# Optimization experiments

Hardware: AMD Instinct MI355X
Metric: run time of the kernel (lower is better)

Reference implementation:

```python
import jax, jax.numpy as jnp
import numpy as np

N, D, S = 8192, 1024, 16
EPS = 1e-5

def setup_inputs() -> dict:
    key = jax.random.key(0)
    ks = jax.random.split(key, 11)
    return {
        "x_t":   jax.random.normal(ks[0], (N, D), dtype=jnp.float32),
        "state": jax.random.normal(ks[1], (N, D, S), dtype=jnp.float32),
        "log_A": jax.random.normal(ks[2], (D, S), dtype=jnp.float32) * 0.1,
        "B":     jax.random.normal(ks[3], (D, S), dtype=jnp.float32) * 0.1,
        "C":     jax.random.normal(ks[4], (D, S), dtype=jnp.float32) * 0.1,
        "Wd":    jax.random.normal(ks[5], (D, D), dtype=jnp.float32) * (1.0 / np.sqrt(D)),
        "bd":    jnp.zeros((D,), dtype=jnp.float32),
        "Wg":    jax.random.normal(ks[6], (D, D), dtype=jnp.float32) * (1.0 / np.sqrt(D)),
        "bg":    jnp.zeros((D,), dtype=jnp.float32),
        "gamma": jnp.ones((D,), dtype=jnp.float32),
        "beta":  jnp.zeros((D,), dtype=jnp.float32),
    }

def reference(x_t, state, log_A, B, C, Wd, bd, Wg, bg, gamma, beta):
    # delta_proj: Linear + Softplus  -> [n, d]
    delta = jax.nn.softplus(x_t @ Wd.T + bd)
    # continuous A and exp discretization -> [n, d, s]
    A_cont = -jnp.exp(log_A)
    A_disc = jnp.exp(delta[:, :, None] * A_cont[None])
    # B_disc * x_t[..., None] == (delta * x_t)[:, :, None] * B
    new_state = A_disc * state + (delta * x_t)[:, :, None] * B[None]
    # contract tiny state dim s=16 -> [n, d]
    out = jnp.einsum('nds,ds->nd', new_state, C)
    gate = jax.nn.silu(x_t @ Wg.T + bg)
    residual = x_t + gate * out
    # LayerNorm (biased variance, eps=1e-5, affine)
    mu = jnp.mean(residual, axis=-1, keepdims=True)
    var = jnp.mean(jnp.square(residual - mu), axis=-1, keepdims=True)
    y = (residual - mu) / jnp.sqrt(var + EPS) * gamma + beta
    return (y, new_state)
```

## Files before the change

kernel.cpp:

```cpp
#include <hip/hip_runtime.h>

#define N_ROWS 8192
#define DIM 1024
#define S_DIM 16

typedef __attribute__((ext_vector_type(8))) __bf16 bf16x8;
typedef __attribute__((ext_vector_type(4))) float f32x4;

__device__ __forceinline__ unsigned short f2bf(float f) {
  union { float f; unsigned u; } v; v.f = f;
  unsigned r = v.u + 0x7FFFu + ((v.u >> 16) & 1u);
  return (unsigned short)(r >> 16);
}
__device__ __forceinline__ float bf2f(unsigned short b) {
  union { unsigned u; float f; } v; v.u = ((unsigned)b) << 16;
  return v.f;
}

__global__ void cvt_bf16_k(const float* __restrict__ src,
                           unsigned short* __restrict__ dst, int n4) {
  int i = blockIdx.x * blockDim.x + threadIdx.x;
  if (i >= n4) return;
  float4 v = ((const float4*)src)[i];
  ushort4 o;
  o.x = f2bf(v.x); o.y = f2bf(v.y); o.z = f2bf(v.z); o.w = f2bf(v.w);
  ((ushort4*)dst)[i] = o;
}

__global__ void acont_k(const float* __restrict__ la, float* __restrict__ ac, int n) {
  int i = blockIdx.x * blockDim.x + threadIdx.x;
  if (i < n) ac[i] = -__expf(la[i]);
}

__global__ __launch_bounds__(256) void gemm_act_k(
    const unsigned short* __restrict__ X,
    const unsigned short* __restrict__ W,
    const float* __restrict__ bias,
    unsigned short* __restrict__ outdg,
    int act)
{
  __shared__ unsigned short As[128][40];
  __shared__ unsigned short Bs[128][40];

  const int tid  = threadIdx.x;
  const int lane = tid & 63;
  const int wave = tid >> 6;
  const int qr = (wave >> 1) * 64;
  const int qc = (wave & 1) * 64;
  const int bj = blockIdx.x * 128;
  const int bn = blockIdx.y * 128;

  f32x4 acc[4][4];
  #pragma unroll
  for (int i = 0; i < 4; i++)
    #pragma unroll
    for (int j = 0; j < 4; j++)
      acc[i][j] = (f32x4){0.f, 0.f, 0.f, 0.f};

  const int sr = tid >> 2;
  const int so = (tid & 3) * 8;
  const unsigned short* Xa = X + (size_t)(bn + sr) * DIM + so;
  const unsigned short* Xb = X + (size_t)(bn + sr + 64) * DIM + so;
  const unsigned short* Wa = W + (size_t)(bj + sr) * DIM + so;
  const unsigned short* Wb = W + (size_t)(bj + sr + 64) * DIM + so;

  const int rl = lane & 15;
  const int kq = (lane >> 4) * 8;

  for (int k0 = 0; k0 < DIM; k0 += 32) {
    int4 a0 = *(const int4*)(Xa + k0);
    int4 a1 = *(const int4*)(Xb + k0);
    int4 b0 = *(const int4*)(Wa + k0);
    int4 b1 = *(const int4*)(Wb + k0);
    __syncthreads();
    *(int4*)&As[sr][so]      = a0;
    *(int4*)&As[sr + 64][so] = a1;
    *(int4*)&Bs[sr][so]      = b0;
    *(int4*)&Bs[sr + 64][so] = b1;
    __syncthreads();

    bf16x8 af[4], bfr[4];
    #pragma unroll
    for (int i = 0; i < 4; i++) af[i]  = *(const bf16x8*)&As[qr + i * 16 + rl][kq];
    #pragma unroll
    for (int j = 0; j < 4; j++) bfr[j] = *(const bf16x8*)&Bs[qc + j * 16 + rl][kq];

    #pragma unroll
    for (int i = 0; i < 4; i++)
      #pragma unroll
      for (int j = 0; j < 4; j++)
        acc[i][j] = __builtin_amdgcn_mfma_f32_16x16x32_bf16(af[i], bfr[j], acc[i][j], 0, 0, 0);
  }

  #pragma unroll
  for (int i = 0; i < 4; i++) {
    const int rowb = bn + qr + i * 16 + (lane >> 4) * 4;
    #pragma unroll
    for (int j = 0; j < 4; j++) {
      const int col = bj + qc + j * 16 + rl;
      const float bia = bias[col];
      #pragma unroll
      for (int r = 0; r < 4; r++) {
        float v = acc[i][j][r] + bia;
        float o;
        if (act == 0) o = (v > 20.f) ? v : log1pf(__expf(v));
        else          o = v / (1.f + __expf(-v));
        outdg[(size_t)(rowb + r) * 2048 + act * 1024 + col] = f2bf(o);
      }
    }
  }
}

__global__ __launch_bounds__(256) void state_ln_k(
    const float* __restrict__ x,
    const float* __restrict__ state,
    const float* __restrict__ acont,
    const float* __restrict__ Bm,
    const float* __restrict__ Cm,
    const float* __restrict__ gamma,
    const float* __restrict__ beta,
    float* __restrict__ y,
    float* __restrict__ ns)
{
  const int n = blockIdx.x;
  const int tid = threadIdx.x;
  const unsigned short* dg = (const unsigned short*)(y + (size_t)n * DIM);

  float res[4];
  #pragma unroll
  for (int q = 0; q < 4; q++) {
    const int d = tid + q * 256;
    const size_t nd = (size_t)n * DIM + d;
    const float xd = x[nd];
    const float dl = bf2f(dg[d]);
    const float gt = bf2f(dg[DIM + d]);
    const float dx = dl * xd;

    const float4* st = (const float4*)(state + nd * S_DIM);
    float4*       no = (float4*)(ns + nd * S_DIM);
    const float4* a4 = (const float4*)(acont + d * S_DIM);
    const float4* b4 = (const float4*)(Bm + d * S_DIM);
    const float4* c4 = (const float4*)(Cm + d * S_DIM);

    float accv = 0.f;
    #pragma unroll
    for (int s = 0; s < 4; s++) {
      float4 sv = st[s], av = a4[s], bv = b4[s], cv = c4[s];
      float4 o;
      o.x = __expf(dl * av.x) * sv.x + dx * bv.x;
      o.y = __expf(dl * av.y) * sv.y + dx * bv.y;
      o.z = __expf(dl * av.z) * sv.z + dx * bv.z;
      o.w = __expf(dl * av.w) * sv.w + dx * bv.w;
      accv += o.x * cv.x + o.y * cv.y + o.z * cv.z + o.w * cv.w;
      no[s] = o;
    }
    res[q] = xd + gt * accv;
  }

  float s1 = res[0] + res[1] + res[2] + res[3];
  float s2 = res[0] * res[0] + res[1] * res[1] + res[2] * res[2] + res[3] * res[3];
  #pragma unroll
  for (int off = 32; off > 0; off >>= 1) {
    s1 += __shfl_down(s1, off, 64);
    s2 += __shfl_down(s2, off, 64);
  }
  __shared__ float red[8];
  if ((tid & 63) == 0) { red[tid >> 6] = s1; red[4 + (tid >> 6)] = s2; }
  __syncthreads();
  const float t1 = red[0] + red[1] + red[2] + red[3];
  const float t2 = red[4] + red[5] + red[6] + red[7];
  const float mu = t1 * (1.f / (float)DIM);
  const float var = t2 * (1.f / (float)DIM) - mu * mu;
  const float rstd = rsqrtf(var + 1e-5f);

  #pragma unroll
  for (int q = 0; q < 4; q++) {
    const int d = tid + q * 256;
    y[(size_t)n * DIM + d] = (res[q] - mu) * rstd * gamma[d] + beta[d];
  }
}

extern "C" void kernel_launch(void* const* d_in, const int* in_sizes, int n_in,
                              void* d_out, int out_size, void* d_ws, size_t ws_size,
                              hipStream_t stream) {
  const float* x     = (const float*)d_in[0];
  const float* state = (const float*)d_in[1];
  const float* logA  = (const float*)d_in[2];
  const float* Bm    = (const float*)d_in[3];
  const float* Cm    = (const float*)d_in[4];
  const float* Wd    = (const float*)d_in[5];
  const float* bd    = (const float*)d_in[6];
  const float* Wg    = (const float*)d_in[7];
  const float* bg    = (const float*)d_in[8];
  const float* gamma = (const float*)d_in[9];
  const float* beta  = (const float*)d_in[10];

  float* y  = (float*)d_out;
  float* ns = (float*)d_out + (size_t)N_ROWS * DIM;

  unsigned short* xb  = (unsigned short*)d_ws;
  unsigned short* wdb = xb + (size_t)N_ROWS * DIM;
  unsigned short* wgb = wdb + (size_t)DIM * DIM;
  float* acont = (float*)(wgb + (size_t)DIM * DIM);

  hipLaunchKernelGGL(cvt_bf16_k, dim3(8192), dim3(256), 0, stream, x, xb, N_ROWS * DIM / 4);
  hipLaunchKernelGGL(cvt_bf16_k, dim3(1024), dim3(256), 0, stream, Wd, wdb, DIM * DIM / 4);
  hipLaunchKernelGGL(cvt_bf16_k, dim3(1024), dim3(256), 0, stream, Wg, wgb, DIM * DIM / 4);
  hipLaunchKernelGGL(acont_k, dim3(64), dim3(256), 0, stream, logA, acont, DIM * S_DIM);

  hipLaunchKernelGGL(gemm_act_k, dim3(8, 64), dim3(256), 0, stream, xb, wdb, bd,
                     (unsigned short*)y, 0);
  hipLaunchKernelGGL(gemm_act_k, dim3(8, 64), dim3(256), 0, stream, xb, wgb, bg,
                     (unsigned short*)y, 1);

  hipLaunchKernelGGL(state_ln_k, dim3(N_ROWS), dim3(256), 0, stream,
                     x, state, acont, Bm, Cm, gamma, beta, y, ns);
}
```

Baseline: 1.259 ms.

## Coalesce state access with four lanes per channel and merge the two GEMM launches

```diff
diff --git a/kernel.cpp b/kernel.cpp
--- a/kernel.cpp
+++ b/kernel.cpp
@@ -35,9 +35,9 @@
 __global__ __launch_bounds__(256) void gemm_act_k(
     const unsigned short* __restrict__ X,
     const unsigned short* __restrict__ W,
-    const float* __restrict__ bias,
-    unsigned short* __restrict__ outdg,
-    int act)
+    const float* __restrict__ bias_d,
+    const float* __restrict__ bias_g,
+    unsigned short* __restrict__ outdg)
 {
   __shared__ unsigned short As[128][40];
   __shared__ unsigned short Bs[128][40];
@@ -49,6 +49,7 @@
   const int qc = (wave & 1) * 64;
   const int bj = blockIdx.x * 128;
   const int bn = blockIdx.y * 128;
+  const int actq = (bj >= 1024);
 
   f32x4 acc[4][4];
   #pragma unroll
@@ -97,15 +98,15 @@
     const int rowb = bn + qr + i * 16 + (lane >> 4) * 4;
     #pragma unroll
     for (int j = 0; j < 4; j++) {
-      const int col = bj + qc + j * 16 + rl;
-      const float bia = bias[col];
+      const int colp = bj + qc + j * 16 + rl;
+      const float bia = actq ? bias_g[colp - 1024] : bias_d[colp];
       #pragma unroll
       for (int r = 0; r < 4; r++) {
         float v = acc[i][j][r] + bia;
         float o;
-        if (act == 0) o = (v > 20.f) ? v : log1pf(__expf(v));
-        else          o = v / (1.f + __expf(-v));
-        outdg[(size_t)(rowb + r) * 2048 + act * 1024 + col] = f2bf(o);
+        if (!actq) o = (v > 20.f) ? v : log1pf(__expf(v));
+        else       o = v / (1.f + __expf(-v));
+        outdg[(size_t)(rowb + r) * 2048 + colp] = f2bf(o);
       }
     }
   }
@@ -126,45 +127,58 @@
   const int tid = threadIdx.x;
   const unsigned short* dg = (const unsigned short*)(y + (size_t)n * DIM);
 
-  float res[4];
-  #pragma unroll
-  for (int q = 0; q < 4; q++) {
-    const int d = tid + q * 256;
+  const int sc  = tid & 3;
+  const int dl4 = tid >> 2;
+
+  __shared__ float rbuf[DIM];
+  __shared__ float red[8];
+
+  const float4* st4 = (const float4*)state;
+  float4*       ns4 = (float4*)ns;
+  const float4* a4  = (const float4*)acont;
+  const float4* b4  = (const float4*)Bm;
+  const float4* c4  = (const float4*)Cm;
+
+  float s1 = 0.f, s2 = 0.f;
+  const float lnmask = (sc == 0) ? 1.f : 0.f;
+
+  #pragma unroll 2
+  for (int q = 0; q < 16; q++) {
+    const int d = q * 64 + dl4;
     const size_t nd = (size_t)n * DIM + d;
+
     const float xd = x[nd];
     const float dl = bf2f(dg[d]);
     const float gt = bf2f(dg[DIM + d]);
     const float dx = dl * xd;
 
-    const float4* st = (const float4*)(state + nd * S_DIM);
-    float4*       no = (float4*)(ns + nd * S_DIM);
-    const float4* a4 = (const float4*)(acont + d * S_DIM);
-    const float4* b4 = (const float4*)(Bm + d * S_DIM);
-    const float4* c4 = (const float4*)(Cm + d * S_DIM);
-
-    float accv = 0.f;
-    #pragma unroll
-    for (int s = 0; s < 4; s++) {
-      float4 sv = st[s], av = a4[s], bv = b4[s], cv = c4[s];
-      float4 o;
-      o.x = __expf(dl * av.x) * sv.x + dx * bv.x;
-      o.y = __expf(dl * av.y) * sv.y + dx * bv.y;
-      o.z = __expf(dl * av.z) * sv.z + dx * bv.z;
-      o.w = __expf(dl * av.w) * sv.w + dx * bv.w;
-      accv += o.x * cv.x + o.y * cv.y + o.z * cv.z + o.w * cv.w;
-      no[s] = o;
-    }
-    res[q] = xd + gt * accv;
-  }
-
-  float s1 = res[0] + res[1] + res[2] + res[3];
-  float s2 = res[0] * res[0] + res[1] * res[1] + res[2] * res[2] + res[3] * res[3];
+    float4 sv = st4[nd * 4 + sc];
+    float4 av = a4[(size_t)d * 4 + sc];
+    float4 bv = b4[(size_t)d * 4 + sc];
+    float4 cv = c4[(size_t)d * 4 + sc];
+
+    float4 o;
+    o.x = __expf(dl * av.x) * sv.x + dx * bv.x;
+    o.y = __expf(dl * av.y) * sv.y + dx * bv.y;
+    o.z = __expf(dl * av.z) * sv.z + dx * bv.z;
+    o.w = __expf(dl * av.w) * sv.w + dx * bv.w;
+    ns4[nd * 4 + sc] = o;
+
+    float part = o.x * cv.x + o.y * cv.y + o.z * cv.z + o.w * cv.w;
+    part += __shfl_xor(part, 1, 64);
+    part += __shfl_xor(part, 2, 64);
+
+    const float r = xd + gt * part;
+    s1 += lnmask * r;
+    s2 += lnmask * r * r;
+    if (sc == 0) rbuf[d] = r;
+  }
+
   #pragma unroll
   for (int off = 32; off > 0; off >>= 1) {
     s1 += __shfl_down(s1, off, 64);
     s2 += __shfl_down(s2, off, 64);
   }
-  __shared__ float red[8];
   if ((tid & 63) == 0) { red[tid >> 6] = s1; red[4 + (tid >> 6)] = s2; }
   __syncthreads();
   const float t1 = red[0] + red[1] + red[2] + red[3];
@@ -176,7 +190,8 @@
   #pragma unroll
   for (int q = 0; q < 4; q++) {
     const int d = tid + q * 256;
-    y[(size_t)n * DIM + d] = (res[q] - mu) * rstd * gamma[d] + beta[d];
+    const float r = rbuf[d];
+    y[(size_t)n * DIM + d] = (r - mu) * rstd * gamma[d] + beta[d];
   }
 }
 
@@ -208,10 +223,8 @@
   hipLaunchKernelGGL(cvt_bf16_k, dim3(1024), dim3(256), 0, stream, Wg, wgb, DIM * DIM / 4);
   hipLaunchKernelGGL(acont_k, dim3(64), dim3(256), 0, stream, logA, acont, DIM * S_DIM);
 
-  hipLaunchKernelGGL(gemm_act_k, dim3(8, 64), dim3(256), 0, stream, xb, wdb, bd,
-                     (unsigned short*)y, 0);
-  hipLaunchKernelGGL(gemm_act_k, dim3(8, 64), dim3(256), 0, stream, xb, wgb, bg,
-                     (unsigned short*)y, 1);
+  hipLaunchKernelGGL(gemm_act_k, dim3(16, 64), dim3(256), 0, stream, xb, wdb, bd, bg,
+                     (unsigned short*)y);
 
   hipLaunchKernelGGL(state_ln_k, dim3(N_ROWS), dim3(256), 0, stream,
                      x, state, acont, Bm, Cm, gamma, beta, y, ns);
```

Result: faster. 1.086 ms (-13.7%).
